# Kernel tuning notes

Hardware: AMD Instinct MI355X
Metric: run time of the kernel (lower is better)

## Reference

```python
import jax, jax.numpy as jnp
import numpy as np

H = 1000   # hidden_size
B = 64     # batch
S = 512    # encoder source length


def setup_inputs() -> dict:
    key = jax.random.key(0)
    ks = jax.random.split(key, 9)
    scale = 0.02
    return {
        "decoder_hidden": jax.random.normal(ks[0], (1, B, H), jnp.float32),
        "context": jax.random.normal(ks[1], (B, S, 2 * H), jnp.float32),
        "mask": jax.random.randint(ks[2], (B, S, 1), 0, 2) == 1,
        "W_a": jax.random.normal(ks[3], (H, 2 * H), jnp.float32) * scale,
        "W_b": jax.random.normal(ks[4], (H, H), jnp.float32) * scale,
        "W_c_w": jax.random.normal(ks[5], (1, H), jnp.float32) * scale,
        "W_c_b": jax.random.normal(ks[6], (1,), jnp.float32) * scale,
        "dense_w": jax.random.normal(ks[7], (H, 2 * H), jnp.float32) * scale,
        "dense_b": jax.random.normal(ks[8], (H,), jnp.float32) * scale,
    }


def reference(decoder_hidden, context, mask, W_a, W_b, W_c_w, W_c_b, dense_w, dense_b):
    # context_in: (B, S, H)
    context_in = jnp.einsum('bsd,hd->bsh', context, W_a)
    # hidden_in: (1, B, H) @ W_b.T -> transpose(0,1) -> (B, 1, H)
    hidden_in = jnp.transpose(jnp.einsum('nbd,hd->nbh', decoder_hidden, W_b), (1, 0, 2))
    # scores: (B, S, 1)
    attention = jnp.einsum('bsh,oh->bso', jnp.tanh(context_in + hidden_in), W_c_w) + W_c_b
    attention = jnp.where(mask, jnp.asarray(-1e6, attention.dtype), attention)
    attention_softmaxed = jax.nn.softmax(attention, axis=1)  # softmax over source length
    # weighted_sum: (B, 1, S) x (B, S, 2H) -> (B, 1, 2H)
    weighted_sum = jnp.einsum('bso,bsd->bod', attention_softmaxed, context)
    # dense: (B, 1, H)
    return jnp.einsum('bod,hd->boh', weighted_sum, dense_w) + dense_b
```

## Files before the change

### kernel.cpp

```cpp
#include <hip/hip_runtime.h>
#include <hip/hip_bf16.h>

#define H 1000
#define B 64
#define S 512
#define D 2000
#define KP 2048
#define NP 1024
#define MP 32768
#define KS 10

typedef __attribute__((ext_vector_type(8))) short short8;
typedef __attribute__((ext_vector_type(4))) float f32x4;
typedef __attribute__((ext_vector_type(16))) float f32x16;

__device__ inline unsigned short f2bf(float f) {
  __hip_bfloat16 h = __float2bfloat16(f);
  union { __hip_bfloat16 h; unsigned short u; } c; c.h = h;
  return c.u;
}
__device__ inline float bf2f(unsigned short u) {
  union { unsigned u; float f; } x; x.u = ((unsigned)u) << 16;
  return x.f;
}
__device__ inline float tanh_fast(float x) {
  float e2 = __expf(2.f * x);
  return 1.f - 2.f / (e2 + 1.f);
}

__global__ __launch_bounds__(256) void k_dect(const float* __restrict__ dec,
                                              float* __restrict__ dec_t) {
  const int d = blockIdx.x * 4 + (threadIdx.x >> 6);
  const int b = threadIdx.x & 63;
  dec_t[d * 64 + b] = dec[b * H + d];
}

__global__ __launch_bounds__(256) void k_hidden2(const float* __restrict__ dec_t,
                                                 const float* __restrict__ Wb,
                                                 float* __restrict__ hi) {
  const int h = blockIdx.x * 4 + (threadIdx.x >> 6);
  const int lane = threadIdx.x & 63;
  const float* w = Wb + (size_t)h * H;
  float acc = 0.f;
#pragma unroll 4
  for (int d = 0; d < H; ++d) acc += w[d] * dec_t[d * 64 + lane];
  hi[lane * H + h] = acc;
}

__global__ __launch_bounds__(256) void k_hidden(const float* __restrict__ dec,
                                                const float* __restrict__ Wb,
                                                float* __restrict__ hi) {
  __shared__ float sdec[H];
  const int b = blockIdx.y;
  const int h = blockIdx.x * 4 + (threadIdx.x >> 6);
  const int lane = threadIdx.x & 63;
  for (int d = threadIdx.x; d < H; d += 256) sdec[d] = dec[b * H + d];
  __syncthreads();
  const float* w = Wb + (size_t)h * H;
  float acc = 0.f;
  for (int d = lane; d < H; d += 64) acc += w[d] * sdec[d];
  for (int o = 32; o; o >>= 1) acc += __shfl_xor(acc, o);
  if (lane == 0) hi[b * H + h] = acc;
}

__global__ __launch_bounds__(256) void k_cvt2(const float* __restrict__ ctx,
                                              const float* __restrict__ wa,
                                              unsigned short* __restrict__ ctx_b,
                                              unsigned short* __restrict__ wa_b) {
  const int bp = blockIdx.x;
  const float* src;
  unsigned short* dst;
  int valid_rows, rp;
  if (bp < 128) { src = ctx; dst = ctx_b; valid_rows = MP; rp = bp; }
  else          { src = wa;  dst = wa_b;  valid_rows = H;  rp = bp - 128; }
  const int tid = threadIdx.x;
  const int r0 = tid >> 2;
  const int kq = tid & 3;
  const int t0 = blockIdx.y * 8;
  for (int tt = 0; tt < 8; ++tt) {
    const int t = t0 + tt;
    const int gcol = t * 32 + kq * 8;
    unsigned short* ob = dst + ((size_t)rp * 64 + t) * 8192;
#pragma unroll
    for (int w = 0; w < 4; ++w) {
      const int grow = rp * 256 + r0 + w * 64;
      unsigned short v[8];
      if (grow < valid_rows && gcol + 8 <= D) {
        const float* p = src + (size_t)grow * D + gcol;
        float4 x = *(const float4*)p;
        float4 y = *(const float4*)(p + 4);
        v[0] = f2bf(x.x); v[1] = f2bf(x.y); v[2] = f2bf(x.z); v[3] = f2bf(x.w);
        v[4] = f2bf(y.x); v[5] = f2bf(y.y); v[6] = f2bf(y.z); v[7] = f2bf(y.w);
      } else {
#pragma unroll
        for (int z = 0; z < 8; ++z) v[z] = 0;
      }
      *(short8*)(ob + (kq * 256 + r0 + w * 64) * 8) = *(short8*)&v[0];
    }
  }
}

__global__ __launch_bounds__(1024) void k_scores_fast(const unsigned short* __restrict__ ctxb,
                                                      const unsigned short* __restrict__ wab,
                                                      const float* __restrict__ hi,
                                                      const float* __restrict__ Wcw,
                                                      float* __restrict__ scores) {
  __shared__ unsigned short As[3][8192];
  __shared__ unsigned short Bs[3][8192];

  const int bid = blockIdx.x;
  const int swz = (bid & 7) * 64 + (bid >> 3);
  const int rtile = swz >> 2;
  const int ctile = swz & 3;
  const int row0 = rtile * 256;
  const int col0 = ctile * 256;

  const int tid = threadIdx.x;
  const int lane = tid & 63;
  const int wid = tid >> 6;
  const int wm = wid >> 2;
  const int wn = wid & 3;
  const int ln31 = lane & 31;
  const int kh = lane >> 5;

  const unsigned short* ga = ctxb + (size_t)rtile * (64 * 8192);
  const unsigned short* gb = wab + (size_t)ctile * (64 * 8192);

  f32x16 acc[2][2];
#pragma unroll
  for (int i = 0; i < 2; ++i)
#pragma unroll
    for (int j = 0; j < 2; ++j)
#pragma unroll
      for (int r = 0; r < 16; ++r) acc[i][j][r] = 0.f;

#define STAGE(T, BUF)                                                                                      \
  do {                                                                                                     \
    const unsigned short* pa = ga + (size_t)(T) * 8192 + tid * 8;                                          \
    const unsigned short* pb = gb + (size_t)(T) * 8192 + tid * 8;                                          \
    __builtin_amdgcn_global_load_lds((const __attribute__((address_space(1))) unsigned int*)pa,            \
                                     (__attribute__((address_space(3))) unsigned int*)&As[BUF][tid * 8],   \
                                     16, 0, 0);                                                            \
    __builtin_amdgcn_global_load_lds((const __attribute__((address_space(1))) unsigned int*)pb,            \
                                     (__attribute__((address_space(3))) unsigned int*)&Bs[BUF][tid * 8],   \
                                     16, 0, 0);                                                            \
  } while (0)

  const int abase = kh * 2048 + (wm * 64 + ln31) * 8;
  const int bbase = kh * 2048 + (wn * 64 + ln31) * 8;

#define COMPUTE(BI)                                                                     \
  do {                                                                                  \
    _Pragma("unroll")                                                                   \
    for (int ks = 0; ks < 2; ++ks) {                                                    \
      short8 a[2], bb[2];                                                               \
      _Pragma("unroll")                                                                 \
      for (int mi = 0; mi < 2; ++mi)                                                    \
        a[mi] = *(const short8*)&As[BI][abase + ks * 4096 + mi * 256];                  \
      _Pragma("unroll")                                                                 \
      for (int ni = 0; ni < 2; ++ni)                                                    \
        bb[ni] = *(const short8*)&Bs[BI][bbase + ks * 4096 + ni * 256];                 \
      __builtin_amdgcn_s_setprio(1);                                                    \
      _Pragma("unroll")                                                                 \
      for (int mi = 0; mi < 2; ++mi)                                                    \
        _Pragma("unroll")                                                               \
        for (int ni = 0; ni < 2; ++ni)                                                  \
          acc[mi][ni] = __builtin_amdgcn_mfma_f32_32x32x16_bf16(a[mi], bb[ni], acc[mi][ni], 0, 0, 0); \
      __builtin_amdgcn_s_setprio(0);                                                    \
    }                                                                                   \
  } while (0)

#define ITER(T, BC, BS)                                      \
  do {                                                       \
    STAGE((T) + 2, BS);                                      \
    COMPUTE(BC);                                             \
    asm volatile("s_waitcnt vmcnt(2)" ::: "memory");         \
    __builtin_amdgcn_s_barrier();                            \
  } while (0)

  STAGE(0, 0);
  STAGE(1, 1);
  asm volatile("s_waitcnt vmcnt(2)" ::: "memory");
  __builtin_amdgcn_s_barrier();

  for (int t = 0; t < 60; t += 3) {
    ITER(t, 0, 2);
    ITER(t + 1, 1, 0);
    ITER(t + 2, 2, 1);
  }
  ITER(60, 0, 2);
  ITER(61, 1, 0);
  COMPUTE(2);
  asm volatile("s_waitcnt vmcnt(0)" ::: "memory");
  __builtin_amdgcn_s_barrier();
  COMPUTE(0);
#undef ITER
#undef STAGE
#undef COMPUTE

  const int b_idx = row0 >> 9;
  float wc[2], hv[2];
#pragma unroll
  for (int ni = 0; ni < 2; ++ni) {
    const int h = col0 + wn * 64 + ni * 32 + ln31;
    wc[ni] = (h < H) ? Wcw[h] : 0.f;
    hv[ni] = (h < H) ? hi[b_idx * H + h] : 0.f;
  }
#pragma unroll
  for (int mi = 0; mi < 2; ++mi) {
#pragma unroll
    for (int reg = 0; reg < 16; ++reg) {
      float p = wc[0] * tanh_fast(acc[mi][0][reg] + hv[0])
              + wc[1] * tanh_fast(acc[mi][1][reg] + hv[1]);
      p += __shfl_xor(p, 1);
      p += __shfl_xor(p, 2);
      p += __shfl_xor(p, 4);
      p += __shfl_xor(p, 8);
      p += __shfl_xor(p, 16);
      if (ln31 == 0) {
        const int n = row0 + wm * 64 + mi * 32 + (reg & 3) + 8 * (reg >> 2) + 4 * kh;
        atomicAdd(&scores[n], p);
      }
    }
  }
}

#define BM 128
#define BN 128
#define BK 32
#define NT 63
__global__ __launch_bounds__(256) void k_scores(const float* __restrict__ ctx,
                                                const float* __restrict__ Wa,
                                                const float* __restrict__ hi,
                                                const float* __restrict__ Wcw,
                                                float* __restrict__ scores) {
  __shared__ unsigned short As[2][BM][BK];
  __shared__ unsigned short Bs[2][BN][BK];

  const int bid = blockIdx.x;
  const int swz = (bid & 7) * 256 + (bid >> 3);
  const int row0 = (swz >> 3) * BM;
  const int col0 = (swz & 7) * BN;

  const int tid = threadIdx.x;
  const int lane = tid & 63;
  const int wid = tid >> 6;
  const int wm = wid >> 1;
  const int wn = wid & 1;
  const int fr = lane & 15;
  const int fq = lane >> 4;

  const int trow = tid >> 1;
  const int thalf = tid & 1;

  f32x4 acc[4][4];
#pragma unroll
  for (int i = 0; i < 4; ++i)
#pragma unroll
    for (int j = 0; j < 4; ++j) acc[i][j] = (f32x4){0.f, 0.f, 0.f, 0.f};

  const float* aptr = ctx + (size_t)(row0 + trow) * D + thalf * 16;
  const int hB = col0 + trow;
  const bool bvalid = (hB < H);
  const float* bptr = Wa + (size_t)(bvalid ? hB : 0) * D + thalf * 16;

  float4 ra[4], rb[4];

#define LOADT(T)                                                     \
  do {                                                               \
    const int base = (T) * BK + thalf * 16;                          \
    _Pragma("unroll")                                                \
    for (int q = 0; q < 4; ++q) {                                    \
      const int kk = base + q * 4;                                   \
      if (kk < D) {                                                  \
        ra[q] = *(const float4*)(aptr + (T) * BK + q * 4);           \
        if (bvalid) rb[q] = *(const float4*)(bptr + (T) * BK + q * 4); \
      }                                                              \
    }                                                                \
  } while (0)

#define CVTW(T, BUF)                                                 \
  do {                                                               \
    const int base = (T) * BK + thalf * 16;                          \
    unsigned short ta[16], tb[16];                                   \
    _Pragma("unroll")                                                \
    for (int q = 0; q < 4; ++q) {                                    \
      const int kk = base + q * 4;                                   \
      const bool v = (kk < D);                                       \
      ta[q * 4 + 0] = v ? f2bf(ra[q].x) : 0;                         \
      ta[q * 4 + 1] = v ? f2bf(ra[q].y) : 0;                         \
      ta[q * 4 + 2] = v ? f2bf(ra[q].z) : 0;                         \
      ta[q * 4 + 3] = v ? f2bf(ra[q].w) : 0;                         \
      const bool vb = v && bvalid;                                   \
      tb[q * 4 + 0] = vb ? f2bf(rb[q].x) : 0;                        \
      tb[q * 4 + 1] = vb ? f2bf(rb[q].y) : 0;                        \
      tb[q * 4 + 2] = vb ? f2bf(rb[q].z) : 0;                        \
      tb[q * 4 + 3] = vb ? f2bf(rb[q].w) : 0;                        \
    }                                                                \
    *(short8*)&As[BUF][trow][thalf * 16]     = *(short8*)&ta[0];     \
    *(short8*)&As[BUF][trow][thalf * 16 + 8] = *(short8*)&ta[8];     \
    *(short8*)&Bs[BUF][trow][thalf * 16]     = *(short8*)&tb[0];     \
    *(short8*)&Bs[BUF][trow][thalf * 16 + 8] = *(short8*)&tb[8];     \
  } while (0)

  LOADT(0);
  CVTW(0, 0);
  LOADT(1);
  __syncthreads();

  int cur = 0;
  for (int t = 0; t < NT; ++t) {
    short8 a[4], bbf[4];
#pragma unroll
    for (int mi = 0; mi < 4; ++mi)
      a[mi] = *(const short8*)&As[cur][wm * 64 + mi * 16 + fr][fq * 8];
#pragma unroll
    for (int ni = 0; ni < 4; ++ni)
      bbf[ni] = *(const short8*)&Bs[cur][wn * 64 + ni * 16 + fr][fq * 8];
#pragma unroll
    for (int mi = 0; mi < 4; ++mi)
#pragma unroll
      for (int ni = 0; ni < 4; ++ni)
        acc[mi][ni] = __builtin_amdgcn_mfma_f32_16x16x32_bf16(a[mi], bbf[ni], acc[mi][ni], 0, 0, 0);

    if (t + 1 < NT) {
      CVTW(t + 1, cur ^ 1);
      if (t + 2 < NT) LOADT(t + 2);
    }
    __syncthreads();
    cur ^= 1;
  }
#undef LOADT
#undef CVTW

  const int b_idx = row0 >> 9;
  float wcv[4], hiv[4];
#pragma unroll
  for (int ni = 0; ni < 4; ++ni) {
    const int h = col0 + wn * 64 + ni * 16 + fr;
    wcv[ni] = (h < H) ? Wcw[h] : 0.f;
    hiv[ni] = (h < H) ? hi[b_idx * H + h] : 0.f;
  }
#pragma unroll
  for (int mi = 0; mi < 4; ++mi) {
#pragma unroll
    for (int r = 0; r < 4; ++r) {
      float p = 0.f;
#pragma unroll
      for (int ni = 0; ni < 4; ++ni)
        p += wcv[ni] * tanhf(acc[mi][ni][r] + hiv[ni]);
      p += __shfl_xor(p, 1);
      p += __shfl_xor(p, 2);
      p += __shfl_xor(p, 4);
      p += __shfl_xor(p, 8);
      if (fr == 0)
        atomicAdd(&scores[row0 + wm * 64 + mi * 16 + fq * 4 + r], p);
    }
  }
}

__global__ __launch_bounds__(256) void k_softmax(const float* __restrict__ scores,
                                                 const int* __restrict__ mask,
                                                 const float* __restrict__ Wcb,
                                                 float* __restrict__ probs) {
  __shared__ float buf[S];
  __shared__ float rbuf[256];
  const int b = blockIdx.x;
  const float bias = Wcb[0];
  float mx = -3.4e38f;
  for (int s = threadIdx.x; s < S; s += 256) {
    float a = mask[b * S + s] ? -1e6f : (scores[b * S + s] + bias);
    buf[s] = a;
    mx = fmaxf(mx, a);
  }
  rbuf[threadIdx.x] = mx;
  __syncthreads();
  for (int w = 128; w > 0; w >>= 1) {
    if (threadIdx.x < w) rbuf[threadIdx.x] = fmaxf(rbuf[threadIdx.x], rbuf[threadIdx.x + w]);
    __syncthreads();
  }
  mx = rbuf[0];
  __syncthreads();
  float sum = 0.f;
  for (int s = threadIdx.x; s < S; s += 256) {
    float e = expf(buf[s] - mx);
    buf[s] = e;
    sum += e;
  }
  rbuf[threadIdx.x] = sum;
  __syncthreads();
  for (int w = 128; w > 0; w >>= 1) {
    if (threadIdx.x < w) rbuf[threadIdx.x] += rbuf[threadIdx.x + w];
    __syncthreads();
  }
  const float inv = 1.f / rbuf[0];
  for (int s = threadIdx.x; s < S; s += 256) probs[b * S + s] = buf[s] * inv;
}

__global__ __launch_bounds__(256) void k_wsum_sm(const unsigned short* __restrict__ ctxb,
                                                 const float* __restrict__ scores,
                                                 const int* __restrict__ mask,
                                                 const float* __restrict__ Wcb,
                                                 float* __restrict__ ws2) {
  __shared__ float sp[S];
  __shared__ float red[8];
  const int t = blockIdx.x;
  const int b = blockIdx.y;
  const int tid = threadIdx.x;
  const int p = tid >> 6;
  const int lane = tid & 63;
  const float bias = Wcb[0];

  float a0 = mask[b * S + tid] ? -1e6f : (scores[b * S + tid] + bias);
  float a1 = mask[b * S + tid + 256] ? -1e6f : (scores[b * S + tid + 256] + bias);
  float m = fmaxf(a0, a1);
#pragma unroll
  for (int o = 32; o; o >>= 1) m = fmaxf(m, __shfl_xor(m, o));
  if (lane == 0) red[p] = m;
  __syncthreads();
  m = fmaxf(fmaxf(red[0], red[1]), fmaxf(red[2], red[3]));
  float e0 = expf(a0 - m), e1 = expf(a1 - m);
  float s = e0 + e1;
#pragma unroll
  for (int o = 32; o; o >>= 1) s += __shfl_xor(s, o);
  if (lane == 0) red[4 + p] = s;
  __syncthreads();
  const float inv = 1.f / (red[4] + red[5] + red[6] + red[7]);
  sp[tid] = e0 * inv;
  sp[tid + 256] = e1 * inv;
  __syncthreads();

  float acc[8];
#pragma unroll
  for (int e = 0; e < 8; ++e) acc[e] = 0.f;
#pragma unroll
  for (int rt = 0; rt < 2; ++rt) {
    const unsigned short* chunk = ctxb + ((size_t)(b * 2 + rt) * 64 + t) * 8192;
#pragma unroll
    for (int half = 0; half < 4; ++half) {
      const int row = half * 64 + lane;
      short8 v = *(const short8*)&chunk[(p * 256 + row) * 8];
      const float pv = sp[rt * 256 + row];
#pragma unroll
      for (int e = 0; e < 8; ++e) acc[e] += pv * bf2f((unsigned short)v[e]);
    }
  }
#pragma unroll
  for (int o = 32; o; o >>= 1)
#pragma unroll
    for (int e = 0; e < 8; ++e) acc[e] += __shfl_xor(acc[e], o);
  const int d0 = t * 32 + p * 8;
  if (lane == 0 && d0 < D) {
#pragma unroll
    for (int e = 0; e < 8; ++e) ws2[(size_t)b * D + d0 + e] = acc[e];
  }
}

__global__ __launch_bounds__(256) void k_wsum(const float* __restrict__ ctx,
                                              const float* __restrict__ probs,
                                              float* __restrict__ ws2) {
  __shared__ float p[S];
  const int b = blockIdx.y;
  const int d = blockIdx.x * 256 + threadIdx.x;
  for (int s = threadIdx.x; s < S; s += 256) p[s] = probs[b * S + s];
  __syncthreads();
  if (d < D) {
    float acc = 0.f;
    for (int s = 0; s < S; ++s) acc += p[s] * ctx[(size_t)(b * S + s) * D + d];
    ws2[b * D + d] = acc;
  }
}

__global__ __launch_bounds__(256) void k_dense_part(const float* __restrict__ ws2,
                                                    const float* __restrict__ Dw,
                                                    float* __restrict__ partial) {
  __shared__ float sw[64][201];
  const int tid = threadIdx.x;
  const int ks = blockIdx.y;
  const int k0 = ks * 200;
  for (int idx = tid; idx < 64 * 200; idx += 256) {
    const int b = idx / 200, k = idx - b * 200;
    sw[b][k] = ws2[(size_t)b * D + k0 + k];
  }
  __syncthreads();
  const int h = blockIdx.x * 4 + (tid >> 6);
  const int lane = tid & 63;
  const float* wrow = Dw + (size_t)h * D + k0;
  float acc = 0.f;
#pragma unroll 8
  for (int k = 0; k < 200; ++k) acc += wrow[k] * sw[lane][k];
  partial[((size_t)ks * 64 + lane) * 1000 + h] = acc;
}

__global__ __launch_bounds__(256) void k_dense_red(const float* __restrict__ partial,
                                                   const float* __restrict__ Db,
                                                   float* __restrict__ out) {
  const int idx = blockIdx.x * 256 + threadIdx.x;
  const int h = idx % 1000;
  float acc = Db[h];
#pragma unroll
  for (int ks = 0; ks < KS; ++ks) acc += partial[(size_t)ks * 64000 + idx];
  out[idx] = acc;
}

__global__ __launch_bounds__(256) void k_dense(const float* __restrict__ ws2,
                                               const float* __restrict__ Dw,
                                               const float* __restrict__ Db,
                                               float* __restrict__ out) {
  __shared__ float v[D];
  const int b = blockIdx.y;
  const int h = blockIdx.x * 256 + threadIdx.x;
  for (int d = threadIdx.x; d < D; d += 256) v[d] = ws2[b * D + d];
  __syncthreads();
  if (h < H) {
    const float* w = Dw + (size_t)h * D;
    float acc = 0.f;
    for (int d = 0; d < D; ++d) acc += w[d] * v[d];
    out[b * H + h] = acc + Db[h];
  }
}

extern "C" void kernel_launch(void* const* d_in, const int* in_sizes, int n_in,
                              void* d_out, int out_size, void* d_ws, size_t ws_size,
                              hipStream_t stream) {
  const float* dec = (const float*)d_in[0];
  const float* ctx = (const float*)d_in[1];
  const int*   mask = (const int*)d_in[2];
  const float* Wa  = (const float*)d_in[3];
  const float* Wb  = (const float*)d_in[4];
  const float* Wcw = (const float*)d_in[5];
  const float* Wcb = (const float*)d_in[6];
  const float* Dw  = (const float*)d_in[7];
  const float* Db  = (const float*)d_in[8];
  float* out = (float*)d_out;

  float* hi     = (float*)d_ws;
  float* scores = hi + B * H;
  float* probs  = scores + B * S;
  float* ws2    = probs + B * S;
  const size_t float_words = (size_t)B * H + 2 * B * S + B * D;
  unsigned short* ctx_b = (unsigned short*)((float*)d_ws + float_words);
  unsigned short* wa_b  = ctx_b + (size_t)MP * KP;
  float* dec_t  = (float*)ctx_b;
  float* partial = (float*)ctx_b;
  const size_t need = float_words * 4 + ((size_t)MP * KP + (size_t)NP * KP) * 2;

  hipMemsetAsync(scores, 0, B * S * sizeof(float), stream);
  if (ws_size >= need) {
    k_dect<<<250, 256, 0, stream>>>(dec, dec_t);
    k_hidden2<<<250, 256, 0, stream>>>(dec_t, Wb, hi);
    k_cvt2<<<dim3(132, 8), 256, 0, stream>>>(ctx, Wa, ctx_b, wa_b);
    k_scores_fast<<<512, 1024, 0, stream>>>(ctx_b, wa_b, hi, Wcw, scores);
    k_wsum_sm<<<dim3(63, B), 256, 0, stream>>>(ctx_b, scores, mask, Wcb, ws2);
    k_dense_part<<<dim3(250, KS), 256, 0, stream>>>(ws2, Dw, partial);
    k_dense_red<<<250, 256, 0, stream>>>(partial, Db, out);
  } else {
    k_hidden<<<dim3(250, B), 256, 0, stream>>>(dec, Wb, hi);
    k_scores<<<2048, 256, 0, stream>>>(ctx, Wa, hi, Wcw, scores);
    k_softmax<<<B, 256, 0, stream>>>(scores, mask, Wcb, probs);
    k_wsum<<<dim3((D + 255) / 256, B), 256, 0, stream>>>(ctx, probs, ws2);
    k_dense<<<dim3((H + 255) / 256, B), 256, 0, stream>>>(ws2, Dw, Db, out);
  }
}
```

Before: 397.7 us.

## Halve GEMM block threads, interleave staged loads with MFMA sub-steps, fuse setup kernels

The scores GEMM block drops from 1024 to 512 threads, so each wave now covers 128 rows with twice the accumulators. Each K-tile is split into four quarter-phases, and each phase issues one global-to-LDS load between LDS reads and an MFMA burst, separated by barriers. The decoder transpose and the zeroing of scores move into extra blocks of the conversion kernel, which removes a separate kernel launch and a memset. The dec_t buffer gets its own workspace region. This uses more registers per thread and adds more barriers per tile.

```diff
diff --git a/kernel.cpp b/kernel.cpp
--- a/kernel.cpp
+++ b/kernel.cpp
@@ -26,13 +26,6 @@
 __device__ inline float tanh_fast(float x) {
   float e2 = __expf(2.f * x);
   return 1.f - 2.f / (e2 + 1.f);
-}
-
-__global__ __launch_bounds__(256) void k_dect(const float* __restrict__ dec,
-                                              float* __restrict__ dec_t) {
-  const int d = blockIdx.x * 4 + (threadIdx.x >> 6);
-  const int b = threadIdx.x & 63;
-  dec_t[d * 64 + b] = dec[b * H + d];
 }
 
 __global__ __launch_bounds__(256) void k_hidden2(const float* __restrict__ dec_t,
@@ -65,9 +58,25 @@
 
 __global__ __launch_bounds__(256) void k_cvt2(const float* __restrict__ ctx,
                                               const float* __restrict__ wa,
+                                              const float* __restrict__ dec,
                                               unsigned short* __restrict__ ctx_b,
-                                              unsigned short* __restrict__ wa_b) {
+                                              unsigned short* __restrict__ wa_b,
+                                              float* __restrict__ dec_t,
+                                              float* __restrict__ scores) {
   const int bp = blockIdx.x;
+  if (bp >= 132) {
+    if (blockIdx.y == 0) {
+      for (int i = threadIdx.x; i < B * H; i += 256) {
+        const int d = i >> 6, b = i & 63;
+        dec_t[i] = dec[b * H + d];
+      }
+    } else if (blockIdx.y == 1) {
+      float4 z = {0.f, 0.f, 0.f, 0.f};
+      float4* sc4 = (float4*)scores;
+      for (int i = threadIdx.x; i < B * S / 4; i += 256) sc4[i] = z;
+    }
+    return;
+  }
   const float* src;
   unsigned short* dst;
   int valid_rows, rp;
@@ -100,11 +109,11 @@
   }
 }
 
-__global__ __launch_bounds__(1024) void k_scores_fast(const unsigned short* __restrict__ ctxb,
-                                                      const unsigned short* __restrict__ wab,
-                                                      const float* __restrict__ hi,
-                                                      const float* __restrict__ Wcw,
-                                                      float* __restrict__ scores) {
+__global__ __launch_bounds__(512) void k_scores_fast(const unsigned short* __restrict__ ctxb,
+                                                     const unsigned short* __restrict__ wab,
+                                                     const float* __restrict__ hi,
+                                                     const float* __restrict__ Wcw,
+                                                     float* __restrict__ scores) {
   __shared__ unsigned short As[3][8192];
   __shared__ unsigned short Bs[3][8192];
 
@@ -126,77 +135,97 @@
   const unsigned short* ga = ctxb + (size_t)rtile * (64 * 8192);
   const unsigned short* gb = wab + (size_t)ctile * (64 * 8192);
 
-  f32x16 acc[2][2];
-#pragma unroll
-  for (int i = 0; i < 2; ++i)
+  f32x16 acc[4][2];
+#pragma unroll
+  for (int i = 0; i < 4; ++i)
 #pragma unroll
     for (int j = 0; j < 2; ++j)
 #pragma unroll
       for (int r = 0; r < 16; ++r) acc[i][j][r] = 0.f;
 
-#define STAGE(T, BUF)                                                                                      \
-  do {                                                                                                     \
-    const unsigned short* pa = ga + (size_t)(T) * 8192 + tid * 8;                                          \
-    const unsigned short* pb = gb + (size_t)(T) * 8192 + tid * 8;                                          \
-    __builtin_amdgcn_global_load_lds((const __attribute__((address_space(1))) unsigned int*)pa,            \
-                                     (__attribute__((address_space(3))) unsigned int*)&As[BUF][tid * 8],   \
-                                     16, 0, 0);                                                            \
-    __builtin_amdgcn_global_load_lds((const __attribute__((address_space(1))) unsigned int*)pb,            \
-                                     (__attribute__((address_space(3))) unsigned int*)&Bs[BUF][tid * 8],   \
-                                     16, 0, 0);                                                            \
+#define GLD(SRC, DST)                                                                       \
+  __builtin_amdgcn_global_load_lds((const __attribute__((address_space(1))) unsigned int*)(SRC), \
+                                   (__attribute__((address_space(3))) unsigned int*)(DST), 16, 0, 0)
+#define SPA0(T, BUF) GLD(ga + (size_t)(T) * 8192 + tid * 8,        &As[BUF][tid * 8])
+#define SPA1(T, BUF) GLD(ga + (size_t)(T) * 8192 + 4096 + tid * 8, &As[BUF][tid * 8 + 4096])
+#define SPB0(T, BUF) GLD(gb + (size_t)(T) * 8192 + tid * 8,        &Bs[BUF][tid * 8])
+#define SPB1(T, BUF) GLD(gb + (size_t)(T) * 8192 + 4096 + tid * 8, &Bs[BUF][tid * 8 + 4096])
+
+  const int abase = kh * 2048 + (wm * 128 + ln31) * 8;
+  const int bbase = kh * 2048 + (wn * 64 + ln31) * 8;
+
+#define MFMA4(M0, M1)                                                                        \
+  __builtin_amdgcn_s_setprio(1);                                                             \
+  acc[M0][0] = __builtin_amdgcn_mfma_f32_32x32x16_bf16(a0, b0, acc[M0][0], 0, 0, 0);         \
+  acc[M0][1] = __builtin_amdgcn_mfma_f32_32x32x16_bf16(a0, b1, acc[M0][1], 0, 0, 0);         \
+  acc[M1][0] = __builtin_amdgcn_mfma_f32_32x32x16_bf16(a1, b0, acc[M1][0], 0, 0, 0);         \
+  acc[M1][1] = __builtin_amdgcn_mfma_f32_32x32x16_bf16(a1, b1, acc[M1][1], 0, 0, 0);         \
+  __builtin_amdgcn_s_setprio(0);
+
+#define ITER(T, BC, BS, DOSTAGE, VMN)                                                        \
+  do {                                                                                       \
+    short8 a0, a1, b0, b1;                                                                   \
+                                                         \
+    a0 = *(const short8*)&As[BC][abase];                                                     \
+    a1 = *(const short8*)&As[BC][abase + 256];                                               \
+    b0 = *(const short8*)&Bs[BC][bbase];                                                     \
+    b1 = *(const short8*)&Bs[BC][bbase + 256];                                               \
+    if (DOSTAGE) SPA0((T) + 2, BS);                                                          \
+    __builtin_amdgcn_s_barrier();                                                            \
+    asm volatile("s_waitcnt lgkmcnt(0)" ::: "memory");                                       \
+    MFMA4(0, 1)                                                                              \
+    __builtin_amdgcn_s_barrier();                                                            \
+                                                                  \
+    a0 = *(const short8*)&As[BC][abase + 512];                                               \
+    a1 = *(const short8*)&As[BC][abase + 768];                                               \
+    if (DOSTAGE) SPA1((T) + 2, BS);                                                          \
+    __builtin_amdgcn_s_barrier();                                                            \
+    asm volatile("s_waitcnt lgkmcnt(0)" ::: "memory");                                       \
+    MFMA4(2, 3)                                                                              \
+    __builtin_amdgcn_s_barrier();                                                            \
+                                                         \
+    a0 = *(const short8*)&As[BC][abase + 4096];                                              \
+    a1 = *(const short8*)&As[BC][abase + 4096 + 256];                                        \
+    b0 = *(const short8*)&Bs[BC][bbase + 4096];                                              \
+    b1 = *(const short8*)&Bs[BC][bbase + 4096 + 256];                                        \
+    if (DOSTAGE) SPB0((T) + 2, BS);                                                          \
+    __builtin_amdgcn_s_barrier();                                                            \
+    asm volatile("s_waitcnt lgkmcnt(0)" ::: "memory");                                       \
+    MFMA4(0, 1)                                                                              \
+    __builtin_amdgcn_s_barrier();                                                            \
+                             \
+    a0 = *(const short8*)&As[BC][abase + 4096 + 512];                                        \
+    a1 = *(const short8*)&As[BC][abase + 4096 + 768];                                        \
+    if (DOSTAGE) SPB1((T) + 2, BS);                                                          \
+    __builtin_amdgcn_s_barrier();                                                            \
+    asm volatile("s_waitcnt lgkmcnt(0)" ::: "memory");                                       \
+    MFMA4(2, 3)                                                                              \
+    if ((VMN) == 4) asm volatile("s_waitcnt vmcnt(4)" ::: "memory");                         \
+    else            asm volatile("s_waitcnt vmcnt(0)" ::: "memory");                         \
+    __builtin_amdgcn_s_barrier();                                                            \
   } while (0)
 
-  const int abase = kh * 2048 + (wm * 64 + ln31) * 8;
-  const int bbase = kh * 2048 + (wn * 64 + ln31) * 8;
-
-#define COMPUTE(BI)                                                                     \
-  do {                                                                                  \
-    _Pragma("unroll")                                                                   \
-    for (int ks = 0; ks < 2; ++ks) {                                                    \
-      short8 a[2], bb[2];                                                               \
-      _Pragma("unroll")                                                                 \
-      for (int mi = 0; mi < 2; ++mi)                                                    \
-        a[mi] = *(const short8*)&As[BI][abase + ks * 4096 + mi * 256];                  \
-      _Pragma("unroll")                                                                 \
-      for (int ni = 0; ni < 2; ++ni)                                                    \
-        bb[ni] = *(const short8*)&Bs[BI][bbase + ks * 4096 + ni * 256];                 \
-      __builtin_amdgcn_s_setprio(1);                                                    \
-      _Pragma("unroll")                                                                 \
-      for (int mi = 0; mi < 2; ++mi)                                                    \
-        _Pragma("unroll")                                                               \
-        for (int ni = 0; ni < 2; ++ni)                                                  \
-          acc[mi][ni] = __builtin_amdgcn_mfma_f32_32x32x16_bf16(a[mi], bb[ni], acc[mi][ni], 0, 0, 0); \
-      __builtin_amdgcn_s_setprio(0);                                                    \
-    }                                                                                   \
-  } while (0)
-
-#define ITER(T, BC, BS)                                      \
-  do {                                                       \
-    STAGE((T) + 2, BS);                                      \
-    COMPUTE(BC);                                             \
-    asm volatile("s_waitcnt vmcnt(2)" ::: "memory");         \
-    __builtin_amdgcn_s_barrier();                            \
-  } while (0)
-
-  STAGE(0, 0);
-  STAGE(1, 1);
-  asm volatile("s_waitcnt vmcnt(2)" ::: "memory");
+  SPA0(0, 0); SPA1(0, 0); SPB0(0, 0); SPB1(0, 0);
+  SPA0(1, 1); SPA1(1, 1); SPB0(1, 1); SPB1(1, 1);
+  asm volatile("s_waitcnt vmcnt(4)" ::: "memory");
   __builtin_amdgcn_s_barrier();
 
   for (int t = 0; t < 60; t += 3) {
-    ITER(t, 0, 2);
-    ITER(t + 1, 1, 0);
-    ITER(t + 2, 2, 1);
-  }
-  ITER(60, 0, 2);
-  ITER(61, 1, 0);
-  COMPUTE(2);
-  asm volatile("s_waitcnt vmcnt(0)" ::: "memory");
-  __builtin_amdgcn_s_barrier();
-  COMPUTE(0);
+    ITER(t, 0, 2, 1, 4);
+    ITER(t + 1, 1, 0, 1, 4);
+    ITER(t + 2, 2, 1, 1, 4);
+  }
+  ITER(60, 0, 2, 1, 4);
+  ITER(61, 1, 0, 1, 4);
+  ITER(62, 2, 1, 0, 0);
+  ITER(63, 0, 1, 0, 0);
 #undef ITER
-#undef STAGE
-#undef COMPUTE
+#undef MFMA4
+#undef SPA0
+#undef SPA1
+#undef SPB0
+#undef SPB1
+#undef GLD
 
   const int b_idx = row0 >> 9;
   float wc[2], hv[2];
@@ -207,7 +236,7 @@
     hv[ni] = (h < H) ? hi[b_idx * H + h] : 0.f;
   }
 #pragma unroll
-  for (int mi = 0; mi < 2; ++mi) {
+  for (int mi = 0; mi < 4; ++mi) {
 #pragma unroll
     for (int reg = 0; reg < 16; ++reg) {
       float p = wc[0] * tanh_fast(acc[mi][0][reg] + hv[0])
@@ -218,7 +247,7 @@
       p += __shfl_xor(p, 8);
       p += __shfl_xor(p, 16);
       if (ln31 == 0) {
-        const int n = row0 + wm * 64 + mi * 32 + (reg & 3) + 8 * (reg >> 2) + 4 * kh;
+        const int n = row0 + wm * 128 + mi * 32 + (reg & 3) + 8 * (reg >> 2) + 4 * kh;
         atomicAdd(&scores[n], p);
       }
     }
@@ -541,20 +570,19 @@
   const size_t float_words = (size_t)B * H + 2 * B * S + B * D;
   unsigned short* ctx_b = (unsigned short*)((float*)d_ws + float_words);
   unsigned short* wa_b  = ctx_b + (size_t)MP * KP;
-  float* dec_t  = (float*)ctx_b;
+  float* dec_t  = (float*)(wa_b + (size_t)NP * KP);
   float* partial = (float*)ctx_b;
-  const size_t need = float_words * 4 + ((size_t)MP * KP + (size_t)NP * KP) * 2;
-
-  hipMemsetAsync(scores, 0, B * S * sizeof(float), stream);
+  const size_t need = float_words * 4 + ((size_t)MP * KP + (size_t)NP * KP) * 2 + (size_t)B * H * 4;
+
   if (ws_size >= need) {
-    k_dect<<<250, 256, 0, stream>>>(dec, dec_t);
+    k_cvt2<<<dim3(133, 8), 256, 0, stream>>>(ctx, Wa, dec, ctx_b, wa_b, dec_t, scores);
     k_hidden2<<<250, 256, 0, stream>>>(dec_t, Wb, hi);
-    k_cvt2<<<dim3(132, 8), 256, 0, stream>>>(ctx, Wa, ctx_b, wa_b);
-    k_scores_fast<<<512, 1024, 0, stream>>>(ctx_b, wa_b, hi, Wcw, scores);
+    k_scores_fast<<<512, 512, 0, stream>>>(ctx_b, wa_b, hi, Wcw, scores);
     k_wsum_sm<<<dim3(63, B), 256, 0, stream>>>(ctx_b, scores, mask, Wcb, ws2);
     k_dense_part<<<dim3(250, KS), 256, 0, stream>>>(ws2, Dw, partial);
     k_dense_red<<<250, 256, 0, stream>>>(partial, Db, out);
   } else {
+    hipMemsetAsync(scores, 0, B * S * sizeof(float), stream);
     k_hidden<<<dim3(250, B), 256, 0, stream>>>(dec, Wb, hi);
     k_scores<<<2048, 256, 0, stream>>>(ctx, Wa, hi, Wcw, scores);
     k_softmax<<<B, 256, 0, stream>>>(scores, mask, Wcb, probs);
```

After: 451.6 us. 1.14x slower.
